# Performance work log

Measured on AMD Instinct MI355X. Metric: run time of the kernel, lower is better.

## Reference

```python
import jax, jax.numpy as jnp
import numpy as np

N_NODES = 100000
N_EDGES = 1600000
IN_FEATS = 48
OUT_FEATS = 48


def setup_inputs() -> dict:
    key = jax.random.key(0)
    k1, k2, k3, k4, k5 = jax.random.split(key, 5)
    feature = jax.random.normal(k1, (N_NODES, IN_FEATS), dtype=jnp.float32)
    # Xavier-uniform init for the linear weight (as in the torch module)
    limit = float(np.sqrt(6.0 / (IN_FEATS + OUT_FEATS)))
    W = jax.random.uniform(k2, (OUT_FEATS, IN_FEATS), minval=-limit, maxval=limit, dtype=jnp.float32)
    b = jax.random.uniform(k3, (OUT_FEATS,), minval=-limit, maxval=limit, dtype=jnp.float32)
    src = jax.random.randint(k4, (N_EDGES,), 0, N_NODES, dtype=jnp.int32)
    dst = jax.random.randint(k5, (N_EDGES,), 0, N_NODES, dtype=jnp.int32)
    return {"feature": feature, "W": W, "b": b, "src": src, "dst": dst}


def reference(feature, W, b, src, dst):
    # copy_src: message m_e = feature[src[e]]  -> [E, F] gather
    msgs = feature[src]
    # mean reduce over in-edges per destination node (nodes with no in-edges get 0)
    sums = jax.ops.segment_sum(msgs, dst, num_segments=N_NODES)  # [N, F]
    deg = jax.ops.segment_sum(jnp.ones((src.shape[0],), dtype=feature.dtype), dst, num_segments=N_NODES)  # [N]
    mean = sums / jnp.maximum(deg, 1.0)[:, None]
    # linear transform: h @ W^T + b
    return mean @ W.T + b
```

## Files before the change

kernel.cpp:

```cpp
#include <hip/hip_runtime.h>

#define N_NODES 100000
#define N_EDGES 1600000
#define FEATS 48
#define BSH 7
#define BUCK 128
#define NB ((N_NODES + BUCK - 1) / BUCK)
#define EPB 8192
#define PBLK ((N_EDGES + EPB - 1) / EPB)
#define CAP 2688
#define NTILE (N_NODES / 16)
#define TBLK ((NTILE + 15) / 16)
#define WTP 49

typedef __attribute__((ext_vector_type(8))) short short8;
typedef __attribute__((ext_vector_type(4))) float f32x4;

__device__ __forceinline__ float bfu(unsigned short u) {
    return __uint_as_float(((unsigned)u) << 16);
}
__device__ __forceinline__ unsigned short f2bf(float f) {
    unsigned u = __float_as_uint(f);
    u += 0x7fffu + ((u >> 16) & 1u);
    return (unsigned short)(u >> 16);
}

__global__ __launch_bounds__(1024) void zero_gcur(int* __restrict__ gcur) {
    int i = blockIdx.x * 1024 + threadIdx.x;
    if (i < NB) gcur[i] = 0;
}

__global__ __launch_bounds__(1024) void fused_scatter_transform(
    const int* __restrict__ src, const int* __restrict__ dst,
    int* __restrict__ gcur, int* __restrict__ packed,
    const float* __restrict__ feature, const float* __restrict__ W,
    unsigned short* __restrict__ tf) {
    __shared__ int hist[NB];
    __shared__ int lbase[NB];
    int tid = threadIdx.x;
    int bid = blockIdx.x;

    if (bid < PBLK) {
        for (int i = tid; i < NB; i += 1024) hist[i] = 0;
        __syncthreads();
        int e0 = bid * EPB;
        int ks[EPB / 1024], pk[EPB / 1024];
#pragma unroll
        for (int i = 0; i < EPB / 1024; ++i) {
            int e = e0 + i * 1024 + tid;
            if (e < N_EDGES) {
                int d = dst[e], s = src[e];
                ks[i] = d >> BSH;
                pk[i] = (s << BSH) | (d & (BUCK - 1));
                atomicAdd(&hist[ks[i]], 1);
            } else ks[i] = -1;
        }
        __syncthreads();
        for (int i = tid; i < NB; i += 1024) {
            int h = hist[i];
            lbase[i] = h ? atomicAdd(&gcur[i], h) : 0;
            hist[i] = 0;
        }
        __syncthreads();
#pragma unroll
        for (int i = 0; i < EPB / 1024; ++i) {
            int k = ks[i];
            if (k >= 0) {
                int pos = lbase[k] + atomicAdd(&hist[k], 1);
                if (pos < CAP)
                    packed[(size_t)k * CAP + pos] = pk[i];
            }
        }
        return;
    }

    int wave = tid >> 6, lane = tid & 63;
    int tile = (bid - PBLK) * 16 + wave;
    if (tile >= NTILE) return;
    int lw = lane & 15, lg = lane >> 4;

    short8 B0[3], B1[3];
#pragma unroll
    for (int t = 0; t < 3; ++t) {
        int o = t * 16 + lw;
        const float* wr = W + (size_t)o * FEATS + lg * 8;
        float4 w0 = *(const float4*)wr;
        float4 w1 = *(const float4*)(wr + 4);
        short8 bb;
        bb[0] = (short)f2bf(w0.x); bb[1] = (short)f2bf(w0.y);
        bb[2] = (short)f2bf(w0.z); bb[3] = (short)f2bf(w0.w);
        bb[4] = (short)f2bf(w1.x); bb[5] = (short)f2bf(w1.y);
        bb[6] = (short)f2bf(w1.z); bb[7] = (short)f2bf(w1.w);
        B0[t] = bb;
        short8 bc = (short8)0;
        if (lg < 2) {
            const float* wr1 = W + (size_t)o * FEATS + 32 + lg * 8;
            float4 v0 = *(const float4*)wr1;
            float4 v1 = *(const float4*)(wr1 + 4);
            bc[0] = (short)f2bf(v0.x); bc[1] = (short)f2bf(v0.y);
            bc[2] = (short)f2bf(v0.z); bc[3] = (short)f2bf(v0.w);
            bc[4] = (short)f2bf(v1.x); bc[5] = (short)f2bf(v1.y);
            bc[6] = (short)f2bf(v1.z); bc[7] = (short)f2bf(v1.w);
        }
        B1[t] = bc;
    }

    int n_row = tile * 16 + lw;
    const float* ar = feature + (size_t)n_row * FEATS + lg * 8;
    float4 a0 = *(const float4*)ar;
    float4 a1 = *(const float4*)(ar + 4);
    short8 A0;
    A0[0] = (short)f2bf(a0.x); A0[1] = (short)f2bf(a0.y);
    A0[2] = (short)f2bf(a0.z); A0[3] = (short)f2bf(a0.w);
    A0[4] = (short)f2bf(a1.x); A0[5] = (short)f2bf(a1.y);
    A0[6] = (short)f2bf(a1.z); A0[7] = (short)f2bf(a1.w);
    short8 A1 = (short8)0;
    if (lg < 2) {
        const float* ar1 = feature + (size_t)n_row * FEATS + 32 + lg * 8;
        float4 c0 = *(const float4*)ar1;
        float4 c1 = *(const float4*)(ar1 + 4);
        A1[0] = (short)f2bf(c0.x); A1[1] = (short)f2bf(c0.y);
        A1[2] = (short)f2bf(c0.z); A1[3] = (short)f2bf(c0.w);
        A1[4] = (short)f2bf(c1.x); A1[5] = (short)f2bf(c1.y);
        A1[6] = (short)f2bf(c1.z); A1[7] = (short)f2bf(c1.w);
    }

#pragma unroll
    for (int t = 0; t < 3; ++t) {
        f32x4 acc = {0.f, 0.f, 0.f, 0.f};
        acc = __builtin_amdgcn_mfma_f32_16x16x32_bf16(A0, B0[t], acc, 0, 0, 0);
        acc = __builtin_amdgcn_mfma_f32_16x16x32_bf16(A1, B1[t], acc, 0, 0, 0);
#pragma unroll
        for (int r = 0; r < 4; ++r) {
            int n_out = tile * 16 + lg * 4 + r;
            tf[(size_t)n_out * FEATS + t * 16 + lw] = f2bf(acc[r]);
        }
    }
}

__global__ __launch_bounds__(512) void sort_gather(
    const unsigned short* __restrict__ tf,
    const int* __restrict__ gcur, const int* __restrict__ packed,
    const float* __restrict__ bias, float* __restrict__ out) {
    __shared__ int segL[CAP];
    __shared__ int eidL[CAP];
    __shared__ int hist[BUCK];
    __shared__ int sc[BUCK];
    __shared__ int offL[BUCK];
    __shared__ int curL[BUCK];
    int tid = threadIdx.x;
    int k = blockIdx.x;
    int c = gcur[k]; if (c > CAP) c = CAP;
    const int4* __restrict__ seg4 = (const int4*)(packed + (size_t)k * CAP);
    int c4 = (c + 3) >> 2;
    for (int i = tid; i < c4; i += 512) ((int4*)segL)[i] = seg4[i];
    if (tid < BUCK) hist[tid] = 0;
    __syncthreads();
    for (int i = tid; i < c; i += 512)
        atomicAdd(&hist[segL[i] & (BUCK - 1)], 1);
    __syncthreads();
    if (tid < BUCK) sc[tid] = hist[tid];
    __syncthreads();
#pragma unroll
    for (int d = 1; d < BUCK; d <<= 1) {
        int x = 0;
        if (tid < BUCK && tid >= d) x = sc[tid - d];
        __syncthreads();
        if (tid < BUCK) sc[tid] += x;
        __syncthreads();
    }
    if (tid < BUCK) {
        int excl = sc[tid] - hist[tid];
        offL[tid] = excl;
        curL[tid] = excl;
    }
    __syncthreads();
    for (int i = tid; i < c; i += 512) {
        int pe = segL[i];
        int pos = atomicAdd(&curL[pe & (BUCK - 1)], 1);
        eidL[pos] = pe >> BSH;
    }
    __syncthreads();

    int wave = tid >> 6, lane = tid & 63;
    int g = lane / 12;
    int sub = lane - g * 12;
    bool act = (g < 5);
    int nbase = k * BUCK;

    for (int nd = wave; nd < BUCK; nd += 8) {
        int gn = nbase + nd;
        if (gn >= N_NODES) continue;
        int cc = hist[nd];
        int oo = offL[nd];
        float a0 = 0.f, a1 = 0.f, a2 = 0.f, a3 = 0.f;
        if (cc > 0) {
            int cm1 = cc - 1;
            for (int i = 0; i < cc; i += 20) {
                int i0 = i + g;       i0 = (i0 < cm1) ? i0 : cm1;
                int i1 = i + 5 + g;   i1 = (i1 < cm1) ? i1 : cm1;
                int i2 = i + 10 + g;  i2 = (i2 < cm1) ? i2 : cm1;
                int i3 = i + 15 + g;  i3 = (i3 < cm1) ? i3 : cm1;
                int s0 = eidL[oo + i0];
                int s1 = eidL[oo + i1];
                int s2 = eidL[oo + i2];
                int s3 = eidL[oo + i3];
                ushort4 u0 = *(const ushort4*)(tf + (size_t)s0 * FEATS + sub * 4);
                ushort4 u1 = *(const ushort4*)(tf + (size_t)s1 * FEATS + sub * 4);
                ushort4 u2 = *(const ushort4*)(tf + (size_t)s2 * FEATS + sub * 4);
                ushort4 u3 = *(const ushort4*)(tf + (size_t)s3 * FEATS + sub * 4);
                if (act && (i + g < cc)) {
                    a0 += bfu(u0.x); a1 += bfu(u0.y); a2 += bfu(u0.z); a3 += bfu(u0.w);
                }
                if (act && (i + 5 + g < cc)) {
                    a0 += bfu(u1.x); a1 += bfu(u1.y); a2 += bfu(u1.z); a3 += bfu(u1.w);
                }
                if (act && (i + 10 + g < cc)) {
                    a0 += bfu(u2.x); a1 += bfu(u2.y); a2 += bfu(u2.z); a3 += bfu(u2.w);
                }
                if (act && (i + 15 + g < cc)) {
                    a0 += bfu(u3.x); a1 += bfu(u3.y); a2 += bfu(u3.z); a3 += bfu(u3.w);
                }
            }
        }
        float s0 = a0 + __shfl(a0, lane + 12) + __shfl(a0, lane + 24)
                      + __shfl(a0, lane + 36) + __shfl(a0, lane + 48);
        float s1 = a1 + __shfl(a1, lane + 12) + __shfl(a1, lane + 24)
                      + __shfl(a1, lane + 36) + __shfl(a1, lane + 48);
        float s2 = a2 + __shfl(a2, lane + 12) + __shfl(a2, lane + 24)
                      + __shfl(a2, lane + 36) + __shfl(a2, lane + 48);
        float s3 = a3 + __shfl(a3, lane + 12) + __shfl(a3, lane + 24)
                      + __shfl(a3, lane + 36) + __shfl(a3, lane + 48);
        if (lane < 12) {
            float inv = 1.0f / fmaxf((float)cc, 1.0f);
            const float4 bv = ((const float4*)bias)[lane];
            float4 t;
            t.x = s0 * inv + bv.x; t.y = s1 * inv + bv.y;
            t.z = s2 * inv + bv.z; t.w = s3 * inv + bv.w;
            ((float4*)(out + (size_t)gn * FEATS))[lane] = t;
        }
    }
}


#define FBSH 6
#define FBUCK 64
#define FNB ((N_NODES + FBUCK - 1) / FBUCK)
#define FB_EPB 8192
#define FB_PBLK ((N_EDGES + FB_EPB - 1) / FB_EPB)

__global__ __launch_bounds__(1024) void fb_zero(int* __restrict__ cnt) {
    int i = blockIdx.x * 1024 + threadIdx.x;
    if (i < FNB) cnt[i] = 0;
}

__global__ __launch_bounds__(256) void fb_count(const int* __restrict__ dst,
                                                int* __restrict__ cnt) {
    __shared__ int hist[FNB];
    int tid = threadIdx.x;
    for (int i = tid; i < FNB; i += 256) hist[i] = 0;
    __syncthreads();
    int e0 = blockIdx.x * FB_EPB;
#pragma unroll
    for (int i = 0; i < FB_EPB / 256; ++i) {
        int e = e0 + i * 256 + tid;
        if (e < N_EDGES) atomicAdd(&hist[dst[e] >> FBSH], 1);
    }
    __syncthreads();
    for (int i = tid; i < FNB; i += 256)
        if (hist[i]) atomicAdd(&cnt[i], hist[i]);
}

__global__ __launch_bounds__(256) void fb_scan(const int* __restrict__ cnt,
                                               int* __restrict__ base,
                                               int* __restrict__ cur) {
    __shared__ int warr[256];
    const int PER = (FNB + 255) / 256;
    int t = threadIdx.x;
    int v[7], s = 0;
#pragma unroll
    for (int j = 0; j < PER; ++j) {
        int i = t * PER + j;
        v[j] = (i < FNB) ? cnt[i] : 0;
        s += v[j];
    }
    warr[t] = s;
    __syncthreads();
    for (int d = 1; d < 256; d <<= 1) {
        int x = (t >= d) ? warr[t - d] : 0;
        __syncthreads();
        warr[t] += x;
        __syncthreads();
    }
    int excl = warr[t] - s;
#pragma unroll
    for (int j = 0; j < PER; ++j) {
        int i = t * PER + j;
        if (i < FNB) { base[i] = excl; cur[i] = excl; }
        excl += v[j];
    }
}

__global__ __launch_bounds__(256) void fb_scatter(const int* __restrict__ src,
                                                  const int* __restrict__ dst,
                                                  int* __restrict__ cur,
                                                  int* __restrict__ packed) {
    __shared__ int hist[FNB];
    __shared__ int lbase[FNB];
    int tid = threadIdx.x;
    for (int i = tid; i < FNB; i += 256) hist[i] = 0;
    __syncthreads();
    int e0 = blockIdx.x * FB_EPB;
#pragma unroll
    for (int i = 0; i < FB_EPB / 256; ++i) {
        int e = e0 + i * 256 + tid;
        if (e < N_EDGES) atomicAdd(&hist[dst[e] >> FBSH], 1);
    }
    __syncthreads();
    for (int i = tid; i < FNB; i += 256) {
        int h = hist[i];
        lbase[i] = h ? atomicAdd(&cur[i], h) : 0;
        hist[i] = 0;
    }
    __syncthreads();
#pragma unroll
    for (int i = 0; i < FB_EPB / 256; ++i) {
        int e = e0 + i * 256 + tid;
        if (e < N_EDGES) {
            int d = dst[e], s = src[e];
            int k = d >> FBSH;
            int pos = lbase[k] + atomicAdd(&hist[k], 1);
            packed[pos] = (s << FBSH) | (d & (FBUCK - 1));
        }
    }
}

__global__ __launch_bounds__(256) void fb_nodesort(
    const int* __restrict__ packed, const int* __restrict__ baseArr,
    const int* __restrict__ cntArr, int* __restrict__ eid,
    int* __restrict__ ncnt, int* __restrict__ noff) {
    __shared__ int hist[FBUCK];
    __shared__ int curL[FBUCK];
    int tid = threadIdx.x;
    int k = blockIdx.x;
    int c = cntArr[k];
    int base = baseArr[k];
    if (tid < FBUCK) hist[tid] = 0;
    __syncthreads();
    const int* __restrict__ seg = packed + base;
    for (int i = tid; i < c; i += 256)
        atomicAdd(&hist[seg[i] & (FBUCK - 1)], 1);
    __syncthreads();
    if (tid < FBUCK) {
        int c0 = hist[tid];
        int incl = c0;
#pragma unroll
        for (int d = 1; d < 64; d <<= 1) {
            int v = __shfl_up(incl, d);
            if (tid >= d) incl += v;
        }
        int excl = incl - c0;
        curL[tid] = excl;
        int gn = k * FBUCK + tid;
        if (gn < N_NODES) { ncnt[gn] = c0; noff[gn] = base + excl; }
    }
    __syncthreads();
    for (int i = tid; i < c; i += 256) {
        int pe = seg[i];
        int pos = base + atomicAdd(&curL[pe & (FBUCK - 1)], 1);
        eid[pos] = pe >> FBSH;
    }
}

__global__ __launch_bounds__(256) void fb_gather(
    const float4* __restrict__ feat4,
    const int* __restrict__ cnt, const int* __restrict__ off,
    const int* __restrict__ eid,
    const float* __restrict__ W, const float* __restrict__ b,
    float* __restrict__ out) {
    __shared__ float Wt[FEATS * WTP];
    __shared__ float meanS[4][FEATS];
    int tid = threadIdx.x;
    for (int i = tid; i < FEATS * FEATS; i += 256) {
        int o = i / FEATS, f = i - o * FEATS;
        Wt[f * WTP + o] = W[i];
    }
    __syncthreads();
    int wave = tid >> 6, lane = tid & 63;
    int n = blockIdx.x * 4 + wave;
    if (n >= N_NODES) return;
    int c = cnt[n];
    int o = off[n];
    int g = lane / 12;
    int sub = lane - g * 12;
    bool act = (g < 5);
    float4 acc = make_float4(0.f, 0.f, 0.f, 0.f);
    if (c > 0) {
        int cm1 = c - 1;
        for (int i = 0; i < c; i += 10) {
            int ia = i + g;      ia = (ia < cm1) ? ia : cm1;
            int ib = i + 5 + g;  ib = (ib < cm1) ? ib : cm1;
            int sa = eid[o + ia];
            int sb = eid[o + ib];
            float4 va = feat4[(size_t)sa * 12 + sub];
            float4 vb = feat4[(size_t)sb * 12 + sub];
            if (act && (i + g < c)) {
                acc.x += va.x; acc.y += va.y; acc.z += va.z; acc.w += va.w;
            }
            if (act && (i + 5 + g < c)) {
                acc.x += vb.x; acc.y += vb.y; acc.z += vb.z; acc.w += vb.w;
            }
        }
    }
    float sx = acc.x + __shfl(acc.x, lane + 12) + __shfl(acc.x, lane + 24)
                     + __shfl(acc.x, lane + 36) + __shfl(acc.x, lane + 48);
    float sy = acc.y + __shfl(acc.y, lane + 12) + __shfl(acc.y, lane + 24)
                     + __shfl(acc.y, lane + 36) + __shfl(acc.y, lane + 48);
    float sz = acc.z + __shfl(acc.z, lane + 12) + __shfl(acc.z, lane + 24)
                     + __shfl(acc.z, lane + 36) + __shfl(acc.z, lane + 48);
    float sw = acc.w + __shfl(acc.w, lane + 12) + __shfl(acc.w, lane + 24)
                     + __shfl(acc.w, lane + 36) + __shfl(acc.w, lane + 48);
    if (lane < 12) {
        float inv = 1.0f / fmaxf((float)c, 1.0f);
        float4 t; t.x = sx * inv; t.y = sy * inv; t.z = sz * inv; t.w = sw * inv;
        ((float4*)&meanS[wave][0])[lane] = t;
    }
    if (lane < FEATS) {
        float r = b[lane];
#pragma unroll
        for (int f = 0; f < FEATS; ++f)
            r += meanS[wave][f] * Wt[f * WTP + lane];
        out[(size_t)n * FEATS + lane] = r;
    }
}

extern "C" void kernel_launch(void* const* d_in, const int* in_sizes, int n_in,
                              void* d_out, int out_size, void* d_ws, size_t ws_size,
                              hipStream_t stream) {
    const float* feature = (const float*)d_in[0];
    const float* W       = (const float*)d_in[1];
    const float* b       = (const float*)d_in[2];
    const int*   src     = (const int*)d_in[3];
    const int*   dst     = (const int*)d_in[4];
    float* out = (float*)d_out;

    const size_t TFI = ((size_t)N_NODES * FEATS + 1) / 2;
    const size_t need_new = (TFI + NB + (size_t)NB * CAP) * sizeof(int);

    if (ws_size >= need_new) {
        int* I = (int*)d_ws;
        unsigned short* tf = (unsigned short*)d_ws;
        int* gcur   = I + TFI;
        int* packed = gcur + NB;
        zero_gcur<<<(NB + 1023) / 1024, 1024, 0, stream>>>(gcur);
        fused_scatter_transform<<<PBLK + TBLK, 1024, 0, stream>>>(
            src, dst, gcur, packed, feature, W, tf);
        sort_gather<<<NB, 512, 0, stream>>>(tf, gcur, packed, b, out);
        return;
    }

    const size_t need_fb = ((size_t)3 * FNB + 2 * (size_t)N_NODES + 2 * (size_t)N_EDGES) * sizeof(int);
    if (ws_size >= need_fb) {
        int* I = (int*)d_ws;
        int* cnt    = I;
        int* base   = I + FNB;
        int* cur    = I + 2 * FNB;
        int* ncnt   = I + 3 * FNB;
        int* noff   = ncnt + N_NODES;
        int* packed = noff + N_NODES;
        int* eid    = packed + N_EDGES;
        fb_zero<<<(FNB + 1023) / 1024, 1024, 0, stream>>>(cnt);
        fb_count  <<<FB_PBLK, 256, 0, stream>>>(dst, cnt);
        fb_scan   <<<1, 256, 0, stream>>>(cnt, base, cur);
        fb_scatter<<<FB_PBLK, 256, 0, stream>>>(src, dst, cur, packed);
        fb_nodesort<<<FNB, 256, 0, stream>>>(packed, base, cnt, eid, ncnt, noff);
        fb_gather<<<(N_NODES + 3) / 4, 256, 0, stream>>>((const float4*)feature,
                                                         ncnt, noff, eid, W, b, out);
    }
}
```

Before: 73.96 us.

## Split transformed features into 16-wide planes and gather per plane

The transform kernel now writes its bf16 output as three planar arrays of 16 features (32 bytes per node) instead of one interleaved 48-feature row. The gather kernel loops over the three planes. In each plane, 8 groups of 8 lanes each load a ushort2 per edge, and the group partials are reduced with xor shuffles. This gives each plane a smaller working set that may fit better in cache, and every lane in the wave now does useful work. In exchange, the per-node edge list is walked three times and three times as many gather requests are issued, each smaller.

```diff
diff --git a/kernel.cpp b/kernel.cpp
--- a/kernel.cpp
+++ b/kernel.cpp
@@ -133,7 +133,7 @@
 #pragma unroll
         for (int r = 0; r < 4; ++r) {
             int n_out = tile * 16 + lg * 4 + r;
-            tf[(size_t)n_out * FEATS + t * 16 + lw] = f2bf(acc[r]);
+            tf[((size_t)t * N_NODES + n_out) * 16 + lw] = f2bf(acc[r]);
         }
     }
 }
@@ -183,61 +183,47 @@
     __syncthreads();
 
     int wave = tid >> 6, lane = tid & 63;
-    int g = lane / 12;
-    int sub = lane - g * 12;
-    bool act = (g < 5);
+    int g8 = lane >> 3;
+    int sub = lane & 7;
     int nbase = k * BUCK;
 
-    for (int nd = wave; nd < BUCK; nd += 8) {
-        int gn = nbase + nd;
-        if (gn >= N_NODES) continue;
-        int cc = hist[nd];
-        int oo = offL[nd];
-        float a0 = 0.f, a1 = 0.f, a2 = 0.f, a3 = 0.f;
-        if (cc > 0) {
-            int cm1 = cc - 1;
-            for (int i = 0; i < cc; i += 20) {
-                int i0 = i + g;       i0 = (i0 < cm1) ? i0 : cm1;
-                int i1 = i + 5 + g;   i1 = (i1 < cm1) ? i1 : cm1;
-                int i2 = i + 10 + g;  i2 = (i2 < cm1) ? i2 : cm1;
-                int i3 = i + 15 + g;  i3 = (i3 < cm1) ? i3 : cm1;
-                int s0 = eidL[oo + i0];
-                int s1 = eidL[oo + i1];
-                int s2 = eidL[oo + i2];
-                int s3 = eidL[oo + i3];
-                ushort4 u0 = *(const ushort4*)(tf + (size_t)s0 * FEATS + sub * 4);
-                ushort4 u1 = *(const ushort4*)(tf + (size_t)s1 * FEATS + sub * 4);
-                ushort4 u2 = *(const ushort4*)(tf + (size_t)s2 * FEATS + sub * 4);
-                ushort4 u3 = *(const ushort4*)(tf + (size_t)s3 * FEATS + sub * 4);
-                if (act && (i + g < cc)) {
-                    a0 += bfu(u0.x); a1 += bfu(u0.y); a2 += bfu(u0.z); a3 += bfu(u0.w);
-                }
-                if (act && (i + 5 + g < cc)) {
-                    a0 += bfu(u1.x); a1 += bfu(u1.y); a2 += bfu(u1.z); a3 += bfu(u1.w);
-                }
-                if (act && (i + 10 + g < cc)) {
-                    a0 += bfu(u2.x); a1 += bfu(u2.y); a2 += bfu(u2.z); a3 += bfu(u2.w);
-                }
-                if (act && (i + 15 + g < cc)) {
-                    a0 += bfu(u3.x); a1 += bfu(u3.y); a2 += bfu(u3.z); a3 += bfu(u3.w);
+#pragma unroll
+    for (int p = 0; p < 3; ++p) {
+        const unsigned short* __restrict__ tb = tf + (size_t)p * N_NODES * 16;
+        for (int nd = wave; nd < BUCK; nd += 8) {
+            int gn = nbase + nd;
+            if (gn >= N_NODES) continue;
+            int cc = hist[nd];
+            int oo = offL[nd];
+            float a0 = 0.f, a1 = 0.f;
+            if (cc > 0) {
+                int cm1 = cc - 1;
+                for (int i = 0; i < cc; i += 24) {
+                    int i0 = i + g8;       int j0 = (i0 < cm1) ? i0 : cm1;
+                    int i1 = i + 8 + g8;   int j1 = (i1 < cm1) ? i1 : cm1;
+                    int i2 = i + 16 + g8;  int j2 = (i2 < cm1) ? i2 : cm1;
+                    int s0 = eidL[oo + j0];
+                    int s1 = eidL[oo + j1];
+                    int s2 = eidL[oo + j2];
+                    ushort2 u0 = *(const ushort2*)(tb + (size_t)s0 * 16 + sub * 2);
+                    ushort2 u1 = *(const ushort2*)(tb + (size_t)s1 * 16 + sub * 2);
+                    ushort2 u2 = *(const ushort2*)(tb + (size_t)s2 * 16 + sub * 2);
+                    if (i0 < cc) { a0 += bfu(u0.x); a1 += bfu(u0.y); }
+                    if (i1 < cc) { a0 += bfu(u1.x); a1 += bfu(u1.y); }
+                    if (i2 < cc) { a0 += bfu(u2.x); a1 += bfu(u2.y); }
                 }
             }
-        }
-        float s0 = a0 + __shfl(a0, lane + 12) + __shfl(a0, lane + 24)
-                      + __shfl(a0, lane + 36) + __shfl(a0, lane + 48);
-        float s1 = a1 + __shfl(a1, lane + 12) + __shfl(a1, lane + 24)
-                      + __shfl(a1, lane + 36) + __shfl(a1, lane + 48);
-        float s2 = a2 + __shfl(a2, lane + 12) + __shfl(a2, lane + 24)
-                      + __shfl(a2, lane + 36) + __shfl(a2, lane + 48);
-        float s3 = a3 + __shfl(a3, lane + 12) + __shfl(a3, lane + 24)
-                      + __shfl(a3, lane + 36) + __shfl(a3, lane + 48);
-        if (lane < 12) {
-            float inv = 1.0f / fmaxf((float)cc, 1.0f);
-            const float4 bv = ((const float4*)bias)[lane];
-            float4 t;
-            t.x = s0 * inv + bv.x; t.y = s1 * inv + bv.y;
-            t.z = s2 * inv + bv.z; t.w = s3 * inv + bv.w;
-            ((float4*)(out + (size_t)gn * FEATS))[lane] = t;
+            a0 += __shfl_xor(a0, 8);  a1 += __shfl_xor(a1, 8);
+            a0 += __shfl_xor(a0, 16); a1 += __shfl_xor(a1, 16);
+            a0 += __shfl_xor(a0, 32); a1 += __shfl_xor(a1, 32);
+            if (lane < 8) {
+                float inv = 1.0f / fmaxf((float)cc, 1.0f);
+                const float2 bv = ((const float2*)bias)[p * 8 + lane];
+                float2 t2;
+                t2.x = a0 * inv + bv.x;
+                t2.y = a1 * inv + bv.y;
+                ((float2*)(out + (size_t)gn * FEATS + p * 16))[lane] = t2;
+            }
         }
     }
 }
```

Measured after the change: 98.35 us. +33.0%, slower.
